# Kernel optimization log

Hardware: AMD Instinct MI355X
Metric: run time of the kernel (lower is better)

The kernel has to match this reference:

```python
import jax, jax.numpy as jnp
import numpy as np

B, S, E, H, D = 8, 1024, 1024, 16, 64
LN_EPS = 1e-5


def setup_inputs() -> dict:
    key = jax.random.key(0)
    ks = jax.random.split(key, 8)
    scale = 1.0 / np.sqrt(E)
    return {
        "query": jax.random.normal(ks[0], (B, S, E), jnp.float32),
        "key": jax.random.normal(ks[1], (B, S, E), jnp.float32),
        "value": jax.random.normal(ks[2], (B, S, E), jnp.float32),
        "self_attn_mask": jax.random.randint(ks[3], (B, S, S), 0, 2) == 1,
        "Wq": jax.random.normal(ks[4], (E, H * D), jnp.float32) * scale,
        "Wk": jax.random.normal(ks[5], (E, H * D), jnp.float32) * scale,
        "Wv": jax.random.normal(ks[6], (E, H * D), jnp.float32) * scale,
        "Wo": jax.random.normal(ks[7], (H * D, E), jnp.float32) * scale,
        "ln_gamma": jnp.ones((E,), jnp.float32),
        "ln_beta": jnp.zeros((E,), jnp.float32),
    }


def reference(query, key, value, self_attn_mask, Wq, Wk, Wv, Wo, ln_gamma, ln_beta):
    identity = query
    # project and split heads: [B, S, E] -> [B, H, S, D]
    q = (query @ Wq).reshape(B, S, H, D).transpose(0, 2, 1, 3)
    k = (key @ Wk).reshape(B, S, H, D).transpose(0, 2, 1, 3)
    v = (value @ Wv).reshape(B, S, H, D).transpose(0, 2, 1, 3)
    # scaled dot-product scores in fp32, additive mask fill -1e9
    score = jnp.einsum("bhsd,bhtd->bhst", q, k).astype(jnp.float32) / np.sqrt(D)
    score = jnp.where(self_attn_mask[:, None, :, :], jnp.float32(-1e9), score)
    attn = jax.nn.softmax(score, axis=-1)
    degree = jnp.einsum("bhst,bhtd->bhsd", attn, v)  # [B, H, S, D]
    degree = degree.transpose(0, 2, 1, 3).reshape(B, S, H * D)
    out = degree @ Wo + identity
    # LayerNorm over last dim
    mu = jnp.mean(out, axis=-1, keepdims=True)
    var = jnp.var(out, axis=-1, keepdims=True)
    out = (out - mu) * jax.lax.rsqrt(var + LN_EPS) * ln_gamma + ln_beta
    return out
```

## Files before the change

kernel.cpp:

```cpp
#include <hip/hip_runtime.h>
#include <hip/hip_bf16.h>
#include <cstdint>
#include <cstddef>

typedef __attribute__((ext_vector_type(8))) short bf16x8;
typedef __attribute__((ext_vector_type(8))) unsigned short ushort8;
typedef __attribute__((ext_vector_type(4))) unsigned short ushort4v;
typedef __attribute__((ext_vector_type(4))) float f32x4;

#define B_ 8
#define S_ 1024
#define E_ 1024
#define H_ 16
#define D_ 64
#define NW_ (S_ / 64)

__device__ __forceinline__ unsigned short f2bf(float f) {
    union { float fp; unsigned int u; } v; v.fp = f;
    unsigned int u = v.u;
    return (unsigned short)((u + 0x7fffu + ((u >> 16) & 1u)) >> 16);
}

__device__ __forceinline__ float fexp2(float x) {
    return __builtin_amdgcn_exp2f(x);
}

__device__ __forceinline__ unsigned cvt_pk_bf16(float lo, float hi) {
    unsigned r;
    asm("v_cvt_pk_bf16_f32 %0, %1, %2" : "=v"(r) : "v"(lo), "v"(hi));
    return r;
}

__device__ __forceinline__ void gload16(const void* g, void* l) {
    __builtin_amdgcn_global_load_lds((__attribute__((address_space(1))) void*)g,
                                     (__attribute__((address_space(3))) void*)l,
                                     16, 0, 0);
}

__global__ __launch_bounds__(256) void wtrans4(const float* __restrict__ W0,
                                               const float* __restrict__ W1,
                                               const float* __restrict__ W2,
                                               const float* __restrict__ W3,
                                               unsigned short* __restrict__ T0,
                                               unsigned short* __restrict__ T1,
                                               unsigned short* __restrict__ T2,
                                               unsigned short* __restrict__ T3) {
    const float* W = (blockIdx.z == 0) ? W0 : (blockIdx.z == 1) ? W1 : (blockIdx.z == 2) ? W2 : W3;
    unsigned short* Wt = (blockIdx.z == 0) ? T0 : (blockIdx.z == 1) ? T1 : (blockIdx.z == 2) ? T2 : T3;
    __shared__ float tile[32][33];
    const int k0 = blockIdx.y * 32, n0 = blockIdx.x * 32;
    const int tx = threadIdx.x & 31, ty = threadIdx.x >> 5;
#pragma unroll
    for (int i = ty; i < 32; i += 8)
        tile[i][tx] = W[(size_t)(k0 + i) * E_ + n0 + tx];
    __syncthreads();
#pragma unroll
    for (int i = ty; i < 32; i += 8)
        Wt[(size_t)(n0 + i) * E_ + k0 + tx] = f2bf(tile[tx][i]);
}

__global__ void detect_kernel(const unsigned int* __restrict__ m, int* __restrict__ flag) {
    unsigned int bad = 0;
    for (int i = threadIdx.x; i < 4096; i += 64) bad |= (m[i] > 1u) ? 1u : 0u;
    unsigned long long anybad = __ballot(bad != 0u);
    if (threadIdx.x == 0) *flag = (anybad == 0ull) ? 1 : 0;
}

__global__ __launch_bounds__(256) void pack_mask(const void* __restrict__ maskp,
                                                 const int* __restrict__ flagp,
                                                 unsigned long long* __restrict__ mbits) {
    const int mask32 = *flagp;
    const int lane = threadIdx.x & 63;
    const int gw = blockIdx.x * 4 + (threadIdx.x >> 6);
    const int nwaves = gridDim.x * 4;
    const int totw = B_ * S_ * NW_;
    for (int w = gw; w < totw; w += nwaves) {
        bool m;
        if (mask32) m = ((const int*)maskp)[(size_t)w * 64 + lane] != 0;
        else        m = ((const unsigned char*)maskp)[(size_t)w * 64 + lane] != 0;
        unsigned long long bits = __ballot(m);
        if (lane == 0) mbits[w] = bits;
    }
}

__global__ __launch_bounds__(256) void qkv_gemm(const float* __restrict__ Aq,
                                                const float* __restrict__ Ak,
                                                const float* __restrict__ Av,
                                                const unsigned short* __restrict__ Wq,
                                                const unsigned short* __restrict__ Wk,
                                                const unsigned short* __restrict__ Wv,
                                                unsigned short* __restrict__ Qh,
                                                unsigned short* __restrict__ Kh,
                                                unsigned short* __restrict__ Vt,
                                                float qscale) {
    __shared__ float Asf[128 * 32];
    __shared__ unsigned short Bs[128 * 32];
    const int z = blockIdx.z;
    const float* A = (z == 0) ? Aq : (z == 1) ? Ak : Av;
    const unsigned short* Bt = (z == 0) ? Wq : (z == 1) ? Wk : Wv;
    unsigned short* Cp = (z == 0) ? Qh : (z == 1) ? Kh : Vt;
    const float cscale = (z == 0) ? qscale : 1.0f;

    const int t = threadIdx.x;
    const int lane = t & 63, w = t >> 6;
    const int wr = w >> 1, wc = w & 1;
    const int l15 = lane & 15, l4 = lane >> 4;
    const int m0 = blockIdx.x * 128, n0 = blockIdx.y * 128;

    const int lr = lane >> 3, lc = lane & 7;
    const float* Ag[4];
#pragma unroll
    for (int g = 0; g < 4; ++g)
        Ag[g] = A + (size_t)(m0 + w * 32 + g * 8 + lr) * E_ + ((lc ^ lr) << 2);
    float* Alf = &Asf[w * 1024];

    const int srow = w * 32 + (lane >> 2);
    const int scol = (lane & 3) * 8;
    const unsigned short* Bg0 = Bt + (size_t)(n0 + srow) * E_ + scol;
    const unsigned short* Bg1 = Bt + (size_t)(n0 + srow + 16) * E_ + scol;
    unsigned short* Bl = &Bs[w * 1024];

    f32x4 acc[4][4];
#pragma unroll
    for (int i = 0; i < 4; ++i)
#pragma unroll
        for (int j = 0; j < 4; ++j) acc[i][j] = (f32x4){0.f, 0.f, 0.f, 0.f};

    const int r7 = l15 & 7;
    const char* AsB = (const char*)Asf;

    for (int kt = 0; kt < E_; kt += 32) {
#pragma unroll
        for (int g = 0; g < 4; ++g) gload16(Ag[g] + kt, Alf + g * 256);
        gload16(Bg0 + kt, Bl);
        gload16(Bg1 + kt, Bl + 512);
        __syncthreads();
        bf16x8 af[4], bfv[4];
#pragma unroll
        for (int mi = 0; mi < 4; ++mi) {
            const int row = wr * 64 + mi * 16 + l15;
            const int s0 = (l4 * 2) ^ r7, s1 = (l4 * 2 + 1) ^ r7;
            f32x4 a0 = *(const f32x4*)(AsB + row * 128 + s0 * 16);
            f32x4 a1 = *(const f32x4*)(AsB + row * 128 + s1 * 16);
            union { unsigned u[4]; bf16x8 v; } pk;
            pk.u[0] = cvt_pk_bf16(a0[0], a0[1]);
            pk.u[1] = cvt_pk_bf16(a0[2], a0[3]);
            pk.u[2] = cvt_pk_bf16(a1[0], a1[1]);
            pk.u[3] = cvt_pk_bf16(a1[2], a1[3]);
            af[mi] = pk.v;
        }
#pragma unroll
        for (int ni = 0; ni < 4; ++ni)
            bfv[ni] = *(const bf16x8*)&Bs[(wc * 64 + ni * 16 + l15) * 32 + l4 * 8];
#pragma unroll
        for (int mi = 0; mi < 4; ++mi)
#pragma unroll
            for (int ni = 0; ni < 4; ++ni)
                acc[mi][ni] =
                    __builtin_amdgcn_mfma_f32_16x16x32_bf16(af[mi], bfv[ni], acc[mi][ni], 0, 0, 0);
        __syncthreads();
    }
#pragma unroll
    for (int mi = 0; mi < 4; ++mi) {
#pragma unroll
        for (int ni = 0; ni < 4; ++ni) {
#pragma unroll
            for (int r = 0; r < 4; ++r) {
                const int m = m0 + wr * 64 + mi * 16 + l4 * 4 + r;
                const int n = n0 + wc * 64 + ni * 16 + l15;
                const float v = acc[mi][ni][r];
                const int b = m >> 10, s = m & 1023, h = n >> 6, d = n & 63;
                if (z != 2)
                    Cp[(((size_t)b * H_ + h) * S_ + s) * D_ + d] = f2bf(v * cscale);
                else
                    Cp[(((size_t)b * H_ + h) * D_ + d) * S_ + s] = f2bf(v);
            }
        }
    }
}

__global__ __launch_bounds__(256) void gemm_out(const unsigned short* __restrict__ A,
                                                const unsigned short* __restrict__ Bt,
                                                float* __restrict__ Cp,
                                                const float* __restrict__ resid) {
    __shared__ unsigned short As[128 * 32];
    __shared__ unsigned short Bs[128 * 32];
    const int t = threadIdx.x;
    const int lane = t & 63, w = t >> 6;
    const int wr = w >> 1, wc = w & 1;
    const int l15 = lane & 15, l4 = lane >> 4;
    const int m0 = blockIdx.x * 128, n0 = blockIdx.y * 128;

    const int srow = w * 32 + (lane >> 2);
    const int scol = (lane & 3) * 8;
    const unsigned short* Ag0 = A + (size_t)(m0 + srow) * E_ + scol;
    const unsigned short* Ag1 = A + (size_t)(m0 + srow + 16) * E_ + scol;
    const unsigned short* Bg0 = Bt + (size_t)(n0 + srow) * E_ + scol;
    const unsigned short* Bg1 = Bt + (size_t)(n0 + srow + 16) * E_ + scol;
    unsigned short* Al = &As[w * 1024];
    unsigned short* Bl = &Bs[w * 1024];

    f32x4 acc[4][4];
#pragma unroll
    for (int i = 0; i < 4; ++i)
#pragma unroll
        for (int j = 0; j < 4; ++j) acc[i][j] = (f32x4){0.f, 0.f, 0.f, 0.f};

    for (int kt = 0; kt < E_; kt += 32) {
        gload16(Ag0 + kt, Al);
        gload16(Ag1 + kt, Al + 512);
        gload16(Bg0 + kt, Bl);
        gload16(Bg1 + kt, Bl + 512);
        __syncthreads();
        bf16x8 af[4], bfv[4];
#pragma unroll
        for (int mi = 0; mi < 4; ++mi)
            af[mi] = *(const bf16x8*)&As[(wr * 64 + mi * 16 + l15) * 32 + l4 * 8];
#pragma unroll
        for (int ni = 0; ni < 4; ++ni)
            bfv[ni] = *(const bf16x8*)&Bs[(wc * 64 + ni * 16 + l15) * 32 + l4 * 8];
#pragma unroll
        for (int mi = 0; mi < 4; ++mi)
#pragma unroll
            for (int ni = 0; ni < 4; ++ni)
                acc[mi][ni] =
                    __builtin_amdgcn_mfma_f32_16x16x32_bf16(af[mi], bfv[ni], acc[mi][ni], 0, 0, 0);
        __syncthreads();
    }
#pragma unroll
    for (int mi = 0; mi < 4; ++mi) {
#pragma unroll
        for (int ni = 0; ni < 4; ++ni) {
#pragma unroll
            for (int r = 0; r < 4; ++r) {
                const int m = m0 + wr * 64 + mi * 16 + l4 * 4 + r;
                const int n = n0 + wc * 64 + ni * 16 + l15;
                const size_t idx = (size_t)m * E_ + n;
                Cp[idx] = acc[mi][ni][r] + resid[idx];
            }
        }
    }
}

__global__ __launch_bounds__(256) void attn_kernel(const unsigned short* __restrict__ Qh,
                                                   const unsigned short* __restrict__ Kh,
                                                   const unsigned short* __restrict__ Vt,
                                                   const unsigned long long* __restrict__ mbits,
                                                   unsigned short* __restrict__ degree) {
    __shared__ unsigned short Ks[64 * 64];
    __shared__ unsigned short Vs[64 * 64];
    __shared__ unsigned short Ps[4 * 16 * 64];
    const int t = threadIdx.x;
    const int lane = t & 63, w = t >> 6;
    const int l15 = lane & 15, l4 = lane >> 4;
    const int bh = blockIdx.y, b = bh >> 4, h = bh & 15;
    const int q0 = blockIdx.x * 64;
    const int myq = q0 + w * 16 + l15;

    const unsigned long long* mrow = mbits + ((size_t)b * S_ + myq) * NW_;

    bf16x8 qf[2];
    {
        const unsigned short* qptr = Qh + ((size_t)bh * S_ + myq) * D_ + l4 * 8;
        qf[0] = *(const bf16x8*)qptr;
        qf[1] = *(const bf16x8*)(qptr + 32);
    }
    f32x4 O[4];
#pragma unroll
    for (int i = 0; i < 4; ++i) O[i] = (f32x4){0.f, 0.f, 0.f, 0.f};
    float mrun = -3e38f, lrun = 0.f;

    const int srow = t >> 2, sch = (t & 3) * 2;
    const int ssw = (srow & 7) << 4;
    char* KsB = (char*)Ks;
    char* VsB = (char*)Vs;
    char* PsB = (char*)Ps + w * 2048;
    const int psw = (l15 & 7) << 4;

    for (int jt = 0; jt < S_; jt += 64) {
        {
            const unsigned short* kg = Kh + ((size_t)bh * S_ + jt + srow) * D_ + sch * 8;
            *(ushort8*)(KsB + srow * 128 + ((sch * 16) ^ ssw)) = *(const ushort8*)kg;
            *(ushort8*)(KsB + srow * 128 + ((sch * 16 + 16) ^ ssw)) = *(const ushort8*)(kg + 8);
            const unsigned short* vg = Vt + ((size_t)bh * D_ + srow) * S_ + jt + sch * 8;
            *(ushort8*)(VsB + srow * 128 + ((sch * 16) ^ ssw)) = *(const ushort8*)vg;
            *(ushort8*)(VsB + srow * 128 + ((sch * 16 + 16) ^ ssw)) = *(const ushort8*)(vg + 8);
        }
        const unsigned long long mw = mrow[jt >> 6];
        __syncthreads();

        f32x4 sacc[4];
#pragma unroll
        for (int i = 0; i < 4; ++i) sacc[i] = (f32x4){0.f, 0.f, 0.f, 0.f};
#pragma unroll
        for (int ni = 0; ni < 4; ++ni) {
            const int row = l15 + ni * 16;
            const int sw = (row & 7) << 4;
            bf16x8 b0 = *(const bf16x8*)(KsB + row * 128 + ((l4 * 16) ^ sw));
            bf16x8 b1 = *(const bf16x8*)(KsB + row * 128 + ((64 + l4 * 16) ^ sw));
            sacc[ni] = __builtin_amdgcn_mfma_f32_16x16x32_bf16(b0, qf[0], sacc[ni], 0, 0, 0);
            sacc[ni] = __builtin_amdgcn_mfma_f32_16x16x32_bf16(b1, qf[1], sacc[ni], 0, 0, 0);
        }

        float m0 = -3e38f;
#pragma unroll
        for (int ni = 0; ni < 4; ++ni) {
#pragma unroll
            for (int r = 0; r < 4; ++r) {
                const int k = ni * 16 + l4 * 4 + r;
                const float s = ((mw >> k) & 1ull) ? -1e9f : sacc[ni][r];
                sacc[ni][r] = s;
                m0 = fmaxf(m0, s);
            }
        }
        m0 = fmaxf(m0, __shfl_xor(m0, 16, 64));
        m0 = fmaxf(m0, __shfl_xor(m0, 32, 64));
        if (!__all(m0 <= mrun + 8.f)) {
            const float mnew = fmaxf(mrun, m0);
            const float corr = fexp2(mrun - mnew);
            lrun *= corr;
#pragma unroll
            for (int df = 0; df < 4; ++df)
#pragma unroll
                for (int r = 0; r < 4; ++r) O[df][r] *= corr;
            mrun = mnew;
        }
        float ps = 0.f;
#pragma unroll
        for (int ni = 0; ni < 4; ++ni) {
            float p0 = fexp2(sacc[ni][0] - mrun);
            float p1 = fexp2(sacc[ni][1] - mrun);
            float p2 = fexp2(sacc[ni][2] - mrun);
            float p3 = fexp2(sacc[ni][3] - mrun);
            ps += (p0 + p1) + (p2 + p3);
            uint2 pw;
            pw.x = cvt_pk_bf16(p0, p1);
            pw.y = cvt_pk_bf16(p2, p3);
            *(uint2*)(PsB + l15 * 128 + ((ni * 32 + l4 * 8) ^ psw)) = pw;
        }
        ps += __shfl_xor(ps, 16, 64);
        ps += __shfl_xor(ps, 32, 64);
        lrun += ps;

        asm volatile("s_waitcnt lgkmcnt(0)" ::: "memory");
        bf16x8 pa0 = *(const bf16x8*)(PsB + l15 * 128 + ((l4 * 16) ^ psw));
        bf16x8 pa1 = *(const bf16x8*)(PsB + l15 * 128 + ((64 + l4 * 16) ^ psw));
#pragma unroll
        for (int df = 0; df < 4; ++df) {
            const int row = l15 + df * 16;
            const int sw = (row & 7) << 4;
            bf16x8 v0 = *(const bf16x8*)(VsB + row * 128 + ((l4 * 16) ^ sw));
            bf16x8 v1 = *(const bf16x8*)(VsB + row * 128 + ((64 + l4 * 16) ^ sw));
            O[df] = __builtin_amdgcn_mfma_f32_16x16x32_bf16(v0, pa0, O[df], 0, 0, 0);
            O[df] = __builtin_amdgcn_mfma_f32_16x16x32_bf16(v1, pa1, O[df], 0, 0, 0);
        }
        __syncthreads();
    }

    const float inv = 1.f / lrun;
#pragma unroll
    for (int df = 0; df < 4; ++df) {
        ushort4v ow;
#pragma unroll
        for (int r = 0; r < 4; ++r) ow[r] = f2bf(O[df][r] * inv);
        const size_t dst = ((size_t)b * S_ + myq) * (size_t)(H_ * D_) +
                           h * 64 + df * 16 + l4 * 4;
        *(ushort4v*)(degree + dst) = ow;
    }
}

__global__ __launch_bounds__(256) void lnorm(float* __restrict__ io,
                                             const float* __restrict__ gamma,
                                             const float* __restrict__ beta) {
    const int row = blockIdx.x;
    const int t = threadIdx.x;
    float4 v = ((const float4*)(io + (size_t)row * E_))[t];
    float s = v.x + v.y + v.z + v.w;
    float q = v.x * v.x + v.y * v.y + v.z * v.z + v.w * v.w;
#pragma unroll
    for (int off = 32; off; off >>= 1) {
        s += __shfl_down(s, off, 64);
        q += __shfl_down(q, off, 64);
    }
    __shared__ float red[8];
    const int wid = t >> 6;
    if ((t & 63) == 0) { red[wid] = s; red[4 + wid] = q; }
    __syncthreads();
    const float ts = red[0] + red[1] + red[2] + red[3];
    const float tq = red[4] + red[5] + red[6] + red[7];
    const float mean = ts * (1.0f / E_);
    const float var = tq * (1.0f / E_) - mean * mean;
    const float rstd = rsqrtf(var + 1e-5f);
    const float4 g = ((const float4*)gamma)[t];
    const float4 bb = ((const float4*)beta)[t];
    v.x = (v.x - mean) * rstd * g.x + bb.x;
    v.y = (v.y - mean) * rstd * g.y + bb.y;
    v.z = (v.z - mean) * rstd * g.z + bb.z;
    v.w = (v.w - mean) * rstd * g.w + bb.w;
    ((float4*)(io + (size_t)row * E_))[t] = v;
}

extern "C" void kernel_launch(void* const* d_in, const int* in_sizes, int n_in,
                              void* d_out, int out_size, void* d_ws, size_t ws_size,
                              hipStream_t stream) {
    const float* query = (const float*)d_in[0];
    const float* key_ = (const float*)d_in[1];
    const float* value = (const float*)d_in[2];
    const void* maskp = d_in[3];
    const float* Wq = (const float*)d_in[4];
    const float* Wk = (const float*)d_in[5];
    const float* Wv = (const float*)d_in[6];
    const float* Wo = (const float*)d_in[7];
    const float* gamma = (const float*)d_in[8];
    const float* beta = (const float*)d_in[9];
    float* out = (float*)d_out;
    char* ws = (char*)d_ws;
    const size_t MB = 1024ull * 1024ull;

    unsigned short* WqT = (unsigned short*)(ws + 0 * MB);
    unsigned short* WkT = (unsigned short*)(ws + 2 * MB);
    unsigned short* WvT = (unsigned short*)(ws + 4 * MB);
    unsigned short* WoT = (unsigned short*)(ws + 6 * MB);
    unsigned short* Qh = (unsigned short*)(ws + 8 * MB);
    unsigned short* Kh = (unsigned short*)(ws + 24 * MB);
    unsigned short* Vt = (unsigned short*)(ws + 40 * MB);
    unsigned short* deg = (unsigned short*)(ws + 56 * MB);
    int* flag = (int*)(ws + 72 * MB);
    unsigned long long* mbits = (unsigned long long*)(ws + 72 * MB + 4096);

    const float qscale = 0.125f * 1.4426950408889634f;

    wtrans4<<<dim3(32, 32, 4), 256, 0, stream>>>(Wq, Wk, Wv, Wo, WqT, WkT, WvT, WoT);
    detect_kernel<<<1, 64, 0, stream>>>((const unsigned int*)maskp, flag);
    pack_mask<<<2048, 256, 0, stream>>>(maskp, flag, mbits);

    qkv_gemm<<<dim3(64, 8, 3), 256, 0, stream>>>(query, key_, value, WqT, WkT, WvT,
                                                 Qh, Kh, Vt, qscale);

    attn_kernel<<<dim3(16, 128), 256, 0, stream>>>(Qh, Kh, Vt, mbits, deg);

    gemm_out<<<dim3(64, 8), 256, 0, stream>>>(deg, WoT, out, query);
    lnorm<<<8192, 256, 0, stream>>>(out, gamma, beta);
}
```

Measured before the change: 248.2 us.

## Prefetch A tile into registers and convert to bf16 before LDS store

In the QKV projection GEMM, the fp32 A tile is no longer copied into LDS by direct global-to-LDS loads and converted by every wave that reads it. Each thread now loads 16 floats of the next k-tile into registers, converts them to bf16 once and writes them to LDS. The next tile's global load is issued after the barrier so it overlaps the MFMA work. This halves A's LDS footprint and removes the repeated conversions, but adds register pressure and drops the XOR swizzle, which may cause LDS bank conflicts on the bf16 reads.

```diff
diff --git a/kernel.cpp b/kernel.cpp
--- a/kernel.cpp
+++ b/kernel.cpp
@@ -93,7 +93,7 @@
                                                 unsigned short* __restrict__ Kh,
                                                 unsigned short* __restrict__ Vt,
                                                 float qscale) {
-    __shared__ float Asf[128 * 32];
+    __shared__ unsigned short As[128 * 32];
     __shared__ unsigned short Bs[128 * 32];
     const int z = blockIdx.z;
     const float* A = (z == 0) ? Aq : (z == 1) ? Ak : Av;
@@ -107,12 +107,9 @@
     const int l15 = lane & 15, l4 = lane >> 4;
     const int m0 = blockIdx.x * 128, n0 = blockIdx.y * 128;
 
-    const int lr = lane >> 3, lc = lane & 7;
-    const float* Ag[4];
-#pragma unroll
-    for (int g = 0; g < 4; ++g)
-        Ag[g] = A + (size_t)(m0 + w * 32 + g * 8 + lr) * E_ + ((lc ^ lr) << 2);
-    float* Alf = &Asf[w * 1024];
+    const int arow = t >> 1, ahalf = t & 1;
+    const float* Agp = A + (size_t)(m0 + arow) * E_ + ahalf * 16;
+    unsigned short* Adst = &As[arow * 32 + ahalf * 16];
 
     const int srow = w * 32 + (lane >> 2);
     const int scol = (lane & 3) * 8;
@@ -126,29 +123,39 @@
 #pragma unroll
         for (int j = 0; j < 4; ++j) acc[i][j] = (f32x4){0.f, 0.f, 0.f, 0.f};
 
-    const int r7 = l15 & 7;
-    const char* AsB = (const char*)Asf;
+    float4 ap0 = ((const float4*)Agp)[0];
+    float4 ap1 = ((const float4*)Agp)[1];
+    float4 ap2 = ((const float4*)Agp)[2];
+    float4 ap3 = ((const float4*)Agp)[3];
 
     for (int kt = 0; kt < E_; kt += 32) {
-#pragma unroll
-        for (int g = 0; g < 4; ++g) gload16(Ag[g] + kt, Alf + g * 256);
         gload16(Bg0 + kt, Bl);
         gload16(Bg1 + kt, Bl + 512);
-        __syncthreads();
+        {
+            union { unsigned u[4]; bf16x8 v; } lo, hi;
+            lo.u[0] = cvt_pk_bf16(ap0.x, ap0.y);
+            lo.u[1] = cvt_pk_bf16(ap0.z, ap0.w);
+            lo.u[2] = cvt_pk_bf16(ap1.x, ap1.y);
+            lo.u[3] = cvt_pk_bf16(ap1.z, ap1.w);
+            hi.u[0] = cvt_pk_bf16(ap2.x, ap2.y);
+            hi.u[1] = cvt_pk_bf16(ap2.z, ap2.w);
+            hi.u[2] = cvt_pk_bf16(ap3.x, ap3.y);
+            hi.u[3] = cvt_pk_bf16(ap3.z, ap3.w);
+            *(bf16x8*)Adst = lo.v;
+            *(bf16x8*)(Adst + 8) = hi.v;
+        }
+        __syncthreads();
+        if (kt + 32 < E_) {
+            const float* An = Agp + kt + 32;
+            ap0 = ((const float4*)An)[0];
+            ap1 = ((const float4*)An)[1];
+            ap2 = ((const float4*)An)[2];
+            ap3 = ((const float4*)An)[3];
+        }
         bf16x8 af[4], bfv[4];
 #pragma unroll
-        for (int mi = 0; mi < 4; ++mi) {
-            const int row = wr * 64 + mi * 16 + l15;
-            const int s0 = (l4 * 2) ^ r7, s1 = (l4 * 2 + 1) ^ r7;
-            f32x4 a0 = *(const f32x4*)(AsB + row * 128 + s0 * 16);
-            f32x4 a1 = *(const f32x4*)(AsB + row * 128 + s1 * 16);
-            union { unsigned u[4]; bf16x8 v; } pk;
-            pk.u[0] = cvt_pk_bf16(a0[0], a0[1]);
-            pk.u[1] = cvt_pk_bf16(a0[2], a0[3]);
-            pk.u[2] = cvt_pk_bf16(a1[0], a1[1]);
-            pk.u[3] = cvt_pk_bf16(a1[2], a1[3]);
-            af[mi] = pk.v;
-        }
+        for (int mi = 0; mi < 4; ++mi)
+            af[mi] = *(const bf16x8*)&As[(wr * 64 + mi * 16 + l15) * 32 + l4 * 8];
 #pragma unroll
         for (int ni = 0; ni < 4; ++ni)
             bfv[ni] = *(const bf16x8*)&Bs[(wc * 64 + ni * 16 + l15) * 32 + l4 * 8];
```

After: 259.4 us. 1.04x slower.
